# Performance work log

Measured on AMD Instinct MI355X. Metric: run time of the kernel, lower is better.

## Reference

```python
import jax, jax.numpy as jnp
import numpy as np

MARGIN = 1.0  # init kwarg 'margin'
N, D = 8192, 128
NUM_CLASSES = 100

def setup_inputs() -> dict:
    key = jax.random.key(0)
    kx, ky = jax.random.split(key)
    x = jax.random.normal(kx, (N, D), dtype=jnp.float32)
    y = jax.random.randint(ky, (N,), 0, NUM_CLASSES, dtype=jnp.int64)
    return {"x": x, "y": y}

def reference(x, y):
    # Squared euclidean pairwise distances: d[i,j] = sum_k (x[i,k] - x[j,k])^2
    # computed via the ||a||^2 + ||b||^2 - 2 a.b expansion to avoid an NxNxD
    # intermediate. Clamp tiny negatives from fp roundoff.
    sq = jnp.sum(x * x, axis=-1)                      # [N]
    d = sq[:, None] + sq[None, :] - 2.0 * (x @ x.T)   # [N, N]
    d = jnp.maximum(d, 0.0)
    same = (y[:, None] == y[None, :]).astype(x.dtype)  # [N, N] positive-pair mask
    # Faithful to the torch module: dissimilar pairs contribute d, similar
    # pairs contribute hinge clamp(margin - d, 0); mean over all N*N pairs.
    loss = jnp.mean((1.0 - same) * d + same * jnp.maximum(MARGIN - d, 0.0))
    return loss
```

## Files before the change

kernel.cpp:

```cpp
#include <hip/hip_runtime.h>


#define N_ROWS 8192
#define DIM    128
#define NCLS   100
#define CAP    224
#define RB     32
#define SCB    1024
#define GBPC   8
#define GRAMB  (NCLS * GBPC)
#define NREP   8

typedef _Float16 half8  __attribute__((ext_vector_type(8)));
typedef _Float16 half4v __attribute__((ext_vector_type(4)));
typedef float    float4v __attribute__((ext_vector_type(4)));

__global__ __launch_bounds__(256) void rank_kernel(
    const int* __restrict__ y, int* __restrict__ cnt, int* __restrict__ rank)
{
    const int tid = threadIdx.x, r = blockIdx.x * 256 + tid;
    __shared__ int lcnt[NCLS], lbase[NCLS];
    if (tid < NCLS) lcnt[tid] = 0;
    __syncthreads();
    const int c = y[r];
    const int intra = atomicAdd(&lcnt[c], 1);
    __syncthreads();
    if (tid < NCLS && lcnt[tid] > 0)
        lbase[tid] = atomicAdd(&cnt[tid], lcnt[tid]);
    __syncthreads();
    rank[r] = lbase[c] + intra;
}

__global__ __launch_bounds__(256) void scan_kernel(
    const float* __restrict__ x, const int* __restrict__ y,
    const int* __restrict__ rank,
    _Float16* __restrict__ gh, float* __restrict__ sqg,
    float* __restrict__ Scol8, float* __restrict__ SQc8)
{
    const int b = blockIdx.x, tid = threadIdx.x;
    const int l = tid & 31, g = tid >> 5;
    const int r = b * 8 + g;
    const int rep = b & (NREP - 1);
    const float4* x4 = (const float4*)x;
    __shared__ float4 colred[256];

    float4 v = x4[r * 32 + l];
    float s = v.x*v.x + v.y*v.y + v.z*v.z + v.w*v.w;
    s += __shfl_xor(s, 1);  s += __shfl_xor(s, 2);  s += __shfl_xor(s, 4);
    s += __shfl_xor(s, 8);  s += __shfl_xor(s, 16);
    const int c = y[r];
    const int p = rank[r];
    if (p < CAP) {
        half4v h;
        h[0] = (_Float16)v.x; h[1] = (_Float16)v.y;
        h[2] = (_Float16)v.z; h[3] = (_Float16)v.w;
        *(half4v*)(gh + (size_t)(c * CAP + p) * DIM + l * 4) = h;
        if (l == 0) sqg[c * CAP + p] = s;
    }
    if (l == 0) atomicAdd(&SQc8[rep * NCLS + c], s);

    colred[tid] = v;
    __syncthreads();
    if (tid < 32) {
        float4 a = colred[tid];
        #pragma unroll
        for (int gg = 1; gg < 8; ++gg) {
            float4 t = colred[tid + 32 * gg];
            a.x += t.x; a.y += t.y; a.z += t.z; a.w += t.w;
        }
        float* dst = Scol8 + rep * DIM;
        atomicAdd(&dst[4 * tid + 0], a.x);
        atomicAdd(&dst[4 * tid + 1], a.y);
        atomicAdd(&dst[4 * tid + 2], a.z);
        atomicAdd(&dst[4 * tid + 3], a.w);
    }
}

__global__ __launch_bounds__(256) void gram_kernel(
    const _Float16* __restrict__ gh, const float* __restrict__ sqg,
    const int* __restrict__ cnt,
    const float* __restrict__ Scol8, const float* __restrict__ SQc8,
    float* __restrict__ Hsum, float* __restrict__ SSsum,
    int* __restrict__ done, float* __restrict__ out)
{
    const int c = blockIdx.x >> 3, qq = blockIdx.x & 7, tid = threadIdx.x;
    __shared__ float wred[8];
    __shared__ int   lastFlag;

    const int mtrue = cnt[c];
    const int m = mtrue < CAP ? mtrue : CAP;
    const int ntiles = (m + 15) >> 4;
    const int ntp = ntiles * (ntiles + 1) / 2;

    const int wave = tid >> 6, lane = tid & 63;
    const int lr = lane & 15, q = lane >> 4;
    float hacc = 0.f, dsum = 0.f;
    const _Float16* base = gh + (size_t)c * CAP * DIM;
    const float* sqb_ = sqg + c * CAP;

    for (int tp = qq * 4 + wave; tp < ntp; tp += 32) {
        int ta = 0, rem = tp;
        while (rem >= ntiles - ta) { rem -= ntiles - ta; ++ta; }
        const int tb = ta + rem;
        const half8* ap = (const half8*)(base + (ta * 16 + lr) * DIM + q * 8);
        const half8* bp = (const half8*)(base + (tb * 16 + lr) * DIM + q * 8);
        float4v acc = {0.f, 0.f, 0.f, 0.f};
        #pragma unroll
        for (int kb = 0; kb < 4; ++kb)
            acc = __builtin_amdgcn_mfma_f32_16x16x32_f16(ap[kb * 4], bp[kb * 4], acc, 0, 0, 0);
        const float w = (ta == tb) ? 1.f : 2.f;
        const int bb = tb * 16 + lr;
        const float sqb = (bb < m) ? sqb_[bb] : 0.f;
        #pragma unroll
        for (int i = 0; i < 4; ++i) {
            const int a = ta * 16 + q * 4 + i;
            if (a < m && bb < m) {
                const float dot = acc[i];
                dsum += w * dot;
                if (a != bb) {
                    float d = fmaxf(sqb_[a] + sqb - 2.f * dot, 0.f);
                    hacc += w * fmaxf(1.f - d, 0.f);
                }
            }
        }
    }
    #pragma unroll
    for (int off = 32; off > 0; off >>= 1) {
        hacc += __shfl_xor(hacc, off);
        dsum += __shfl_xor(dsum, off);
    }
    if (lane == 0) { wred[wave] = hacc; wred[4 + wave] = dsum; }
    __syncthreads();
    if (tid == 0) {
        float h = wred[0] + wred[1] + wred[2] + wred[3];
        float d = wred[4] + wred[5] + wred[6] + wred[7];
        if (h != 0.f) atomicAdd(Hsum, h);
        if (d != 0.f) atomicAdd(SSsum, d);
        __threadfence();
        int p = atomicAdd(done, 1);
        lastFlag = (p == GRAMB - 1);
    }
    __syncthreads();
    if (!lastFlag) return;

    __threadfence();
    const double Nf = (double)N_ROWS;
    double contrib = 0.0;
    if (tid < DIM) {
        float sc = 0.f;
        #pragma unroll
        for (int k = 0; k < NREP; ++k) sc += Scol8[k * DIM + tid];
        contrib -= 2.0 * (double)sc * (double)sc;
    }
    if (tid < NCLS) {
        float qv = 0.f;
        #pragma unroll
        for (int k = 0; k < NREP; ++k) qv += SQc8[k * NCLS + tid];
        contrib += 2.0 * (double)qv * (Nf - (double)cnt[tid]);
    }
    if (tid == 0) {
        float H  = __hip_atomic_load(Hsum,  __ATOMIC_RELAXED, __HIP_MEMORY_SCOPE_AGENT);
        float SS = __hip_atomic_load(SSsum, __ATOMIC_RELAXED, __HIP_MEMORY_SCOPE_AGENT);
        contrib += 2.0 * (double)SS + (double)H + Nf * 1.0 ;
    }
    __shared__ double dred[256];
    dred[tid] = contrib;
    __syncthreads();
    for (int s = 128; s > 0; s >>= 1) {
        if (tid < s) dred[tid] += dred[tid + s];
        __syncthreads();
    }
    if (tid == 0) out[0] = (float)(dred[0] / (Nf * Nf));
}

extern "C" void kernel_launch(void* const* d_in, const int* in_sizes, int n_in,
                              void* d_out, int out_size, void* d_ws, size_t ws_size,
                              hipStream_t stream) {
    const float* x = (const float*)d_in[0];
    const int*   y = (const int*)d_in[1];

    _Float16* gh = (_Float16*)d_ws;
    float* sqg   = (float*)(gh + (size_t)NCLS * CAP * DIM);
    int*   rank  = (int*)(sqg + NCLS * CAP);
    float* Scol8 = (float*)(rank + N_ROWS);
    float* SQc8  = Scol8 + NREP * DIM;
    float* Hsum  = SQc8 + NREP * NCLS;
    float* SSsum = Hsum + 1;
    int*   cnt   = (int*)(SSsum + 1);
    int*   done  = cnt + NCLS;
    const size_t zero_words = NREP * DIM + NREP * NCLS + 2 + NCLS + 1;

    hipMemsetAsync(Scol8, 0, zero_words * sizeof(float), stream);
    rank_kernel<<<RB,    256, 0, stream>>>(y, cnt, rank);
    scan_kernel<<<SCB,   256, 0, stream>>>(x, y, rank, gh, sqg, Scol8, SQc8);
    gram_kernel<<<GRAMB, 256, 0, stream>>>(gh, sqg, cnt, Scol8, SQc8,
                                           Hsum, SSsum, done, (float*)d_out);
}
```

Measured before the change: 97.74 us.

## Fuse rank, scan and gram kernels into one persistent kernel with grid barrier

Merges the three launches into a single 512-block kernel. Each block ranks 16 rows locally, writes them into per-class fp16 buffers, then waits at a software grid barrier before computing per-class Gram tile pairs, with the work spread across 2000 waves (20 per class). This removes two kernel launch gaps and the separate rank pass. In exchange it relies on all 512 blocks being co-resident for the spin barrier, and it changes how work is split in the Gram phase.

```diff
diff --git a/kernel.cpp b/kernel.cpp
--- a/kernel.cpp
+++ b/kernel.cpp
@@ -5,61 +5,69 @@
 #define DIM    128
 #define NCLS   100
 #define CAP    224
-#define RB     32
-#define SCB    1024
-#define GBPC   8
-#define GRAMB  (NCLS * GBPC)
+#define NBLK   512
 #define NREP   8
 
 typedef _Float16 half8  __attribute__((ext_vector_type(8)));
 typedef _Float16 half4v __attribute__((ext_vector_type(4)));
 typedef float    float4v __attribute__((ext_vector_type(4)));
 
-__global__ __launch_bounds__(256) void rank_kernel(
-    const int* __restrict__ y, int* __restrict__ cnt, int* __restrict__ rank)
-{
-    const int tid = threadIdx.x, r = blockIdx.x * 256 + tid;
-    __shared__ int lcnt[NCLS], lbase[NCLS];
-    if (tid < NCLS) lcnt[tid] = 0;
-    __syncthreads();
-    const int c = y[r];
-    const int intra = atomicAdd(&lcnt[c], 1);
-    __syncthreads();
-    if (tid < NCLS && lcnt[tid] > 0)
-        lbase[tid] = atomicAdd(&cnt[tid], lcnt[tid]);
-    __syncthreads();
-    rank[r] = lbase[c] + intra;
-}
-
-__global__ __launch_bounds__(256) void scan_kernel(
+__global__ __launch_bounds__(256, 2) void fused_kernel(
     const float* __restrict__ x, const int* __restrict__ y,
-    const int* __restrict__ rank,
     _Float16* __restrict__ gh, float* __restrict__ sqg,
-    float* __restrict__ Scol8, float* __restrict__ SQc8)
+    float* __restrict__ Scol8, float* __restrict__ SQc8,
+    float* __restrict__ Hsum, float* __restrict__ SSsum,
+    int* __restrict__ cnt, int* __restrict__ doneA, int* __restrict__ doneB,
+    float* __restrict__ out)
 {
     const int b = blockIdx.x, tid = threadIdx.x;
     const int l = tid & 31, g = tid >> 5;
-    const int r = b * 8 + g;
+    const int r0 = b * 16;
     const int rep = b & (NREP - 1);
+
+    __shared__ int   ycls[16], intra[16];
+    __shared__ int   lcnt[NCLS], lbase[NCLS];
+    __shared__ float4 colred[256];
+    __shared__ float wred[8];
+    __shared__ int   lastFlag;
+
     const float4* x4 = (const float4*)x;
-    __shared__ float4 colred[256];
-
-    float4 v = x4[r * 32 + l];
-    float s = v.x*v.x + v.y*v.y + v.z*v.z + v.w*v.w;
-    s += __shfl_xor(s, 1);  s += __shfl_xor(s, 2);  s += __shfl_xor(s, 4);
-    s += __shfl_xor(s, 8);  s += __shfl_xor(s, 16);
-    const int c = y[r];
-    const int p = rank[r];
-    if (p < CAP) {
-        half4v h;
-        h[0] = (_Float16)v.x; h[1] = (_Float16)v.y;
-        h[2] = (_Float16)v.z; h[3] = (_Float16)v.w;
-        *(half4v*)(gh + (size_t)(c * CAP + p) * DIM + l * 4) = h;
-        if (l == 0) sqg[c * CAP + p] = s;
-    }
-    if (l == 0) atomicAdd(&SQc8[rep * NCLS + c], s);
-
-    colred[tid] = v;
+    float4 v0 = x4[(r0 + g) * 32 + l];
+    float4 v1 = x4[(r0 + 8 + g) * 32 + l];
+
+    if (tid < NCLS) lcnt[tid] = 0;
+    if (tid < 16)   ycls[tid] = y[r0 + tid];
+    __syncthreads();
+    if (tid < 16)   intra[tid] = atomicAdd(&lcnt[ycls[tid]], 1);
+    __syncthreads();
+    if (tid < NCLS && lcnt[tid] > 0)
+        lbase[tid] = atomicAdd(&cnt[tid], lcnt[tid]);
+    __syncthreads();
+
+    float s0 = v0.x*v0.x + v0.y*v0.y + v0.z*v0.z + v0.w*v0.w;
+    float s1 = v1.x*v1.x + v1.y*v1.y + v1.z*v1.z + v1.w*v1.w;
+    #pragma unroll
+    for (int off = 1; off < 32; off <<= 1) {
+        s0 += __shfl_xor(s0, off);
+        s1 += __shfl_xor(s1, off);
+    }
+    const int c0 = ycls[g],     p0 = lbase[c0] + intra[g];
+    const int c1 = ycls[8 + g], p1 = lbase[c1] + intra[8 + g];
+    if (p0 < CAP) {
+        half4v h; h[0]=(_Float16)v0.x; h[1]=(_Float16)v0.y; h[2]=(_Float16)v0.z; h[3]=(_Float16)v0.w;
+        *(half4v*)(gh + (size_t)(c0 * CAP + p0) * DIM + l * 4) = h;
+        if (l == 0) sqg[c0 * CAP + p0] = s0;
+    }
+    if (p1 < CAP) {
+        half4v h; h[0]=(_Float16)v1.x; h[1]=(_Float16)v1.y; h[2]=(_Float16)v1.z; h[3]=(_Float16)v1.w;
+        *(half4v*)(gh + (size_t)(c1 * CAP + p1) * DIM + l * 4) = h;
+        if (l == 0) sqg[c1 * CAP + p1] = s1;
+    }
+    if (l == 0) {
+        atomicAdd(&SQc8[rep * NCLS + c0], s0);
+        atomicAdd(&SQc8[rep * NCLS + c1], s1);
+    }
+    colred[tid] = make_float4(v0.x+v1.x, v0.y+v1.y, v0.z+v1.z, v0.w+v1.w);
     __syncthreads();
     if (tid < 32) {
         float4 a = colred[tid];
@@ -74,52 +82,54 @@
         atomicAdd(&dst[4 * tid + 2], a.z);
         atomicAdd(&dst[4 * tid + 3], a.w);
     }
-}
-
-__global__ __launch_bounds__(256) void gram_kernel(
-    const _Float16* __restrict__ gh, const float* __restrict__ sqg,
-    const int* __restrict__ cnt,
-    const float* __restrict__ Scol8, const float* __restrict__ SQc8,
-    float* __restrict__ Hsum, float* __restrict__ SSsum,
-    int* __restrict__ done, float* __restrict__ out)
-{
-    const int c = blockIdx.x >> 3, qq = blockIdx.x & 7, tid = threadIdx.x;
-    __shared__ float wred[8];
-    __shared__ int   lastFlag;
-
-    const int mtrue = cnt[c];
+
+    __threadfence();
+    __syncthreads();
+    if (tid == 0) {
+        __hip_atomic_fetch_add(doneA, 1, __ATOMIC_RELEASE, __HIP_MEMORY_SCOPE_AGENT);
+        while (__hip_atomic_load(doneA, __ATOMIC_ACQUIRE, __HIP_MEMORY_SCOPE_AGENT) < NBLK)
+            __builtin_amdgcn_s_sleep(8);
+    }
+    __syncthreads();
+    __threadfence();
+
+    const int wave = tid >> 6, lane = tid & 63;
+    const int lr = lane & 15, q = lane >> 4;
+    const int W = b * 4 + wave;
+    const int c = W % 100, k = W / 100;
+    float hacc = 0.f, dsum = 0.f;
+
+    const int mtrue = __hip_atomic_load(&cnt[c], __ATOMIC_RELAXED, __HIP_MEMORY_SCOPE_AGENT);
     const int m = mtrue < CAP ? mtrue : CAP;
     const int ntiles = (m + 15) >> 4;
     const int ntp = ntiles * (ntiles + 1) / 2;
-
-    const int wave = tid >> 6, lane = tid & 63;
-    const int lr = lane & 15, q = lane >> 4;
-    float hacc = 0.f, dsum = 0.f;
     const _Float16* base = gh + (size_t)c * CAP * DIM;
     const float* sqb_ = sqg + c * CAP;
 
-    for (int tp = qq * 4 + wave; tp < ntp; tp += 32) {
-        int ta = 0, rem = tp;
-        while (rem >= ntiles - ta) { rem -= ntiles - ta; ++ta; }
-        const int tb = ta + rem;
-        const half8* ap = (const half8*)(base + (ta * 16 + lr) * DIM + q * 8);
-        const half8* bp = (const half8*)(base + (tb * 16 + lr) * DIM + q * 8);
-        float4v acc = {0.f, 0.f, 0.f, 0.f};
-        #pragma unroll
-        for (int kb = 0; kb < 4; ++kb)
-            acc = __builtin_amdgcn_mfma_f32_16x16x32_f16(ap[kb * 4], bp[kb * 4], acc, 0, 0, 0);
-        const float w = (ta == tb) ? 1.f : 2.f;
-        const int bb = tb * 16 + lr;
-        const float sqb = (bb < m) ? sqb_[bb] : 0.f;
-        #pragma unroll
-        for (int i = 0; i < 4; ++i) {
-            const int a = ta * 16 + q * 4 + i;
-            if (a < m && bb < m) {
-                const float dot = acc[i];
-                dsum += w * dot;
-                if (a != bb) {
-                    float d = fmaxf(sqb_[a] + sqb - 2.f * dot, 0.f);
-                    hacc += w * fmaxf(1.f - d, 0.f);
+    if (k < 20) {
+        for (int tp = k; tp < ntp; tp += 20) {
+            int ta = 0, rem = tp;
+            while (rem >= ntiles - ta) { rem -= ntiles - ta; ++ta; }
+            const int tb = ta + rem;
+            const half8* ap = (const half8*)(base + (ta * 16 + lr) * DIM + q * 8);
+            const half8* bp = (const half8*)(base + (tb * 16 + lr) * DIM + q * 8);
+            float4v acc = {0.f, 0.f, 0.f, 0.f};
+            #pragma unroll
+            for (int kb = 0; kb < 4; ++kb)
+                acc = __builtin_amdgcn_mfma_f32_16x16x32_f16(ap[kb * 4], bp[kb * 4], acc, 0, 0, 0);
+            const float w = (ta == tb) ? 1.f : 2.f;
+            const int bb = tb * 16 + lr;
+            const float sqb = (bb < m) ? sqb_[bb] : 0.f;
+            #pragma unroll
+            for (int i = 0; i < 4; ++i) {
+                const int a = ta * 16 + q * 4 + i;
+                if (a < m && bb < m) {
+                    const float dot = acc[i];
+                    dsum += w * dot;
+                    if (a != bb) {
+                        float d = fmaxf(sqb_[a] + sqb - 2.f * dot, 0.f);
+                        hacc += w * fmaxf(1.f - d, 0.f);
+                    }
                 }
             }
         }
@@ -137,8 +147,8 @@
         if (h != 0.f) atomicAdd(Hsum, h);
         if (d != 0.f) atomicAdd(SSsum, d);
         __threadfence();
-        int p = atomicAdd(done, 1);
-        lastFlag = (p == GRAMB - 1);
+        int p = __hip_atomic_fetch_add(doneB, 1, __ATOMIC_ACQ_REL, __HIP_MEMORY_SCOPE_AGENT);
+        lastFlag = (p == NBLK - 1);
     }
     __syncthreads();
     if (!lastFlag) return;
@@ -149,14 +159,15 @@
     if (tid < DIM) {
         float sc = 0.f;
         #pragma unroll
-        for (int k = 0; k < NREP; ++k) sc += Scol8[k * DIM + tid];
+        for (int kk = 0; kk < NREP; ++kk) sc += Scol8[kk * DIM + tid];
         contrib -= 2.0 * (double)sc * (double)sc;
     }
     if (tid < NCLS) {
         float qv = 0.f;
         #pragma unroll
-        for (int k = 0; k < NREP; ++k) qv += SQc8[k * NCLS + tid];
-        contrib += 2.0 * (double)qv * (Nf - (double)cnt[tid]);
+        for (int kk = 0; kk < NREP; ++kk) qv += SQc8[kk * NCLS + tid];
+        int nc = __hip_atomic_load(&cnt[tid], __ATOMIC_RELAXED, __HIP_MEMORY_SCOPE_AGENT);
+        contrib += 2.0 * (double)qv * (Nf - (double)nc);
     }
     if (tid == 0) {
         float H  = __hip_atomic_load(Hsum,  __ATOMIC_RELAXED, __HIP_MEMORY_SCOPE_AGENT);
@@ -181,18 +192,17 @@
 
     _Float16* gh = (_Float16*)d_ws;
     float* sqg   = (float*)(gh + (size_t)NCLS * CAP * DIM);
-    int*   rank  = (int*)(sqg + NCLS * CAP);
-    float* Scol8 = (float*)(rank + N_ROWS);
+    float* Scol8 = sqg + NCLS * CAP;
     float* SQc8  = Scol8 + NREP * DIM;
     float* Hsum  = SQc8 + NREP * NCLS;
     float* SSsum = Hsum + 1;
     int*   cnt   = (int*)(SSsum + 1);
-    int*   done  = cnt + NCLS;
-    const size_t zero_words = NREP * DIM + NREP * NCLS + 2 + NCLS + 1;
+    int*   doneA = cnt + NCLS;
+    int*   doneB = doneA + 1;
+    const size_t zero_words = NREP * DIM + NREP * NCLS + 2 + NCLS + 2;
 
     hipMemsetAsync(Scol8, 0, zero_words * sizeof(float), stream);
-    rank_kernel<<<RB,    256, 0, stream>>>(y, cnt, rank);
-    scan_kernel<<<SCB,   256, 0, stream>>>(x, y, rank, gh, sqg, Scol8, SQc8);
-    gram_kernel<<<GRAMB, 256, 0, stream>>>(gh, sqg, cnt, Scol8, SQc8,
-                                           Hsum, SSsum, done, (float*)d_out);
+    fused_kernel<<<NBLK, 256, 0, stream>>>(x, y, gh, sqg, Scol8, SQc8,
+                                           Hsum, SSsum, cnt, doneA, doneB,
+                                           (float*)d_out);
 }
```

After: 194.5 us. +99.0%, slower.

## Fold memset into single-block rank kernel and process two rows per scan thread

Applied to the files above, without the earlier changes.

Removes the hipMemsetAsync by zeroing the accumulator region inside a single 1024-thread rank kernel. That kernel counts classes in shared memory and computes ranks through a prefix scan instead of global atomics across 32 blocks. The scan kernel now handles 16 rows per block with half as many blocks and stages labels and ranks in shared memory. This cuts one launch and some atomics, at the cost of serialising the rank pass onto a single block.

```diff
diff --git a/kernel.cpp b/kernel.cpp
--- a/kernel.cpp
+++ b/kernel.cpp
@@ -5,30 +5,49 @@
 #define DIM    128
 #define NCLS   100
 #define CAP    224
-#define RB     32
-#define SCB    1024
+#define SCB    512
 #define GBPC   8
 #define GRAMB  (NCLS * GBPC)
 #define NREP   8
+#define ZWORDS (NREP * DIM + NREP * NCLS + 3)
 
 typedef _Float16 half8  __attribute__((ext_vector_type(8)));
 typedef _Float16 half4v __attribute__((ext_vector_type(4)));
 typedef float    float4v __attribute__((ext_vector_type(4)));
 
-__global__ __launch_bounds__(256) void rank_kernel(
-    const int* __restrict__ y, int* __restrict__ cnt, int* __restrict__ rank)
+__global__ __launch_bounds__(1024) void rank_kernel(
+    const int* __restrict__ y, int* __restrict__ cnt, int* __restrict__ rank,
+    float* __restrict__ zregion)
 {
-    const int tid = threadIdx.x, r = blockIdx.x * 256 + tid;
-    __shared__ int lcnt[NCLS], lbase[NCLS];
+    const int tid = threadIdx.x;
+    __shared__ int lcnt[NCLS], lbase[NCLS], pfx[128];
+
+    for (int i = tid; i < ZWORDS; i += 1024) zregion[i] = 0.f;
     if (tid < NCLS) lcnt[tid] = 0;
     __syncthreads();
-    const int c = y[r];
-    const int intra = atomicAdd(&lcnt[c], 1);
-    __syncthreads();
-    if (tid < NCLS && lcnt[tid] > 0)
-        lbase[tid] = atomicAdd(&cnt[tid], lcnt[tid]);
-    __syncthreads();
-    rank[r] = lbase[c] + intra;
+
+    int yv[8], ord[8];
+    #pragma unroll
+    for (int k = 0; k < 8; ++k) yv[k] = y[tid + k * 1024];
+    #pragma unroll
+    for (int k = 0; k < 8; ++k) ord[k] = atomicAdd(&lcnt[yv[k]], 1);
+    __syncthreads();
+
+    if (tid < NCLS) cnt[tid] = lcnt[tid];
+    if (tid < 128)  pfx[tid] = (tid < NCLS) ? lcnt[tid] : 0;
+    __syncthreads();
+    for (int off = 1; off < 128; off <<= 1) {
+        int v = 0;
+        if (tid < 128) { v = pfx[tid]; if (tid >= off) v += pfx[tid - off]; }
+        __syncthreads();
+        if (tid < 128) pfx[tid] = v;
+        __syncthreads();
+    }
+    if (tid < NCLS) lbase[tid] = pfx[tid] - lcnt[tid];
+    __syncthreads();
+    #pragma unroll
+    for (int k = 0; k < 8; ++k)
+        rank[tid + k * 1024] = lbase[yv[k]] + ord[k];
 }
 
 __global__ __launch_bounds__(256) void scan_kernel(
@@ -39,27 +58,41 @@
 {
     const int b = blockIdx.x, tid = threadIdx.x;
     const int l = tid & 31, g = tid >> 5;
-    const int r = b * 8 + g;
+    const int r0 = b * 16;
     const int rep = b & (NREP - 1);
     const float4* x4 = (const float4*)x;
+    __shared__ int    ycls[16], rnk[16];
     __shared__ float4 colred[256];
 
-    float4 v = x4[r * 32 + l];
-    float s = v.x*v.x + v.y*v.y + v.z*v.z + v.w*v.w;
-    s += __shfl_xor(s, 1);  s += __shfl_xor(s, 2);  s += __shfl_xor(s, 4);
-    s += __shfl_xor(s, 8);  s += __shfl_xor(s, 16);
-    const int c = y[r];
-    const int p = rank[r];
-    if (p < CAP) {
-        half4v h;
-        h[0] = (_Float16)v.x; h[1] = (_Float16)v.y;
-        h[2] = (_Float16)v.z; h[3] = (_Float16)v.w;
-        *(half4v*)(gh + (size_t)(c * CAP + p) * DIM + l * 4) = h;
-        if (l == 0) sqg[c * CAP + p] = s;
-    }
-    if (l == 0) atomicAdd(&SQc8[rep * NCLS + c], s);
-
-    colred[tid] = v;
+    float4 v0 = x4[(r0 + g) * 32 + l];
+    float4 v1 = x4[(r0 + 8 + g) * 32 + l];
+    if (tid < 16) { ycls[tid] = y[r0 + tid]; rnk[tid] = rank[r0 + tid]; }
+
+    float s0 = v0.x*v0.x + v0.y*v0.y + v0.z*v0.z + v0.w*v0.w;
+    float s1 = v1.x*v1.x + v1.y*v1.y + v1.z*v1.z + v1.w*v1.w;
+    #pragma unroll
+    for (int off = 1; off < 32; off <<= 1) {
+        s0 += __shfl_xor(s0, off);
+        s1 += __shfl_xor(s1, off);
+    }
+    __syncthreads();
+    const int c0 = ycls[g],     p0 = rnk[g];
+    const int c1 = ycls[8 + g], p1 = rnk[8 + g];
+    if (p0 < CAP) {
+        half4v h; h[0]=(_Float16)v0.x; h[1]=(_Float16)v0.y; h[2]=(_Float16)v0.z; h[3]=(_Float16)v0.w;
+        *(half4v*)(gh + (size_t)(c0 * CAP + p0) * DIM + l * 4) = h;
+        if (l == 0) sqg[c0 * CAP + p0] = s0;
+    }
+    if (p1 < CAP) {
+        half4v h; h[0]=(_Float16)v1.x; h[1]=(_Float16)v1.y; h[2]=(_Float16)v1.z; h[3]=(_Float16)v1.w;
+        *(half4v*)(gh + (size_t)(c1 * CAP + p1) * DIM + l * 4) = h;
+        if (l == 0) sqg[c1 * CAP + p1] = s1;
+    }
+    if (l == 0) {
+        atomicAdd(&SQc8[rep * NCLS + c0], s0);
+        atomicAdd(&SQc8[rep * NCLS + c1], s1);
+    }
+    colred[tid] = make_float4(v0.x+v1.x, v0.y+v1.y, v0.z+v1.z, v0.w+v1.w);
     __syncthreads();
     if (tid < 32) {
         float4 a = colred[tid];
@@ -186,13 +219,11 @@
     float* SQc8  = Scol8 + NREP * DIM;
     float* Hsum  = SQc8 + NREP * NCLS;
     float* SSsum = Hsum + 1;
-    int*   cnt   = (int*)(SSsum + 1);
-    int*   done  = cnt + NCLS;
-    const size_t zero_words = NREP * DIM + NREP * NCLS + 2 + NCLS + 1;
-
-    hipMemsetAsync(Scol8, 0, zero_words * sizeof(float), stream);
-    rank_kernel<<<RB,    256, 0, stream>>>(y, cnt, rank);
-    scan_kernel<<<SCB,   256, 0, stream>>>(x, y, rank, gh, sqg, Scol8, SQc8);
-    gram_kernel<<<GRAMB, 256, 0, stream>>>(gh, sqg, cnt, Scol8, SQc8,
-                                           Hsum, SSsum, done, (float*)d_out);
-}
+    int*   done  = (int*)(SSsum + 1);
+    int*   cnt   = done + 1;
+
+    rank_kernel<<<1,     1024, 0, stream>>>(y, cnt, rank, Scol8);
+    scan_kernel<<<SCB,   256,  0, stream>>>(x, y, rank, gh, sqg, Scol8, SQc8);
+    gram_kernel<<<GRAMB, 256,  0, stream>>>(gh, sqg, cnt, Scol8, SQc8,
+                                            Hsum, SSsum, done, (float*)d_out);
+}
```

Result: slower. 103.4 us (+5.8%).
